# Optimization experiments

Measured on AMD Instinct MI355X. Metric: run time of the kernel, lower is better.

## Reference

```python
import jax, jax.numpy as jnp
import numpy as np

# Static problem sizes
REC = [5, 3, 6, 2]          # agents per scene (record_len), sum = 16
LMAX = max(REC)              # max cav count per group (static for padding)
C, H, W = 256, 96, 288       # feature channels and BEV spatial dims


def setup_inputs() -> dict:
    key = jax.random.key(0)
    total = sum(REC)
    x = jax.random.normal(key, (total, C, H, W), dtype=jnp.float32)
    record_len = jnp.array(REC, dtype=jnp.int32)
    return {"x": x, "record_len": record_len}


def _att_fusion(x, record_len):
    # x: (sum_cav, C, H, W); record_len: (B,)
    B = record_len.shape[0]
    Cdim, Hh, Ww = x.shape[1], x.shape[2], x.shape[3]
    P = Hh * Ww
    scale = 1.0 / np.sqrt(Cdim)

    # Pad ragged groups to (B, LMAX): row index into x, clamped + masked
    offsets = jnp.concatenate([jnp.zeros((1,), record_len.dtype),
                               jnp.cumsum(record_len)[:-1]])
    l = jnp.arange(LMAX)
    mask = l[None, :] < record_len[:, None]                       # (B, L)
    idx = offsets[:, None] + jnp.minimum(l[None, :], record_len[:, None] - 1)
    xf = x[idx].reshape(B, LMAX, Cdim, P)                         # (B, L, C, P)

    # Only the ego row (token 0) of the per-pixel self-attention is kept,
    # so compute attention for that single query per spatial location.
    q = xf[:, 0]                                                  # (B, C, P)
    scores = jnp.einsum('bcp,blcp->blp', q, xf) * scale           # (B, L, P)
    scores = jnp.where(mask[:, :, None], scores, jnp.float32(-1e9))
    attn = jax.nn.softmax(scores, axis=1)                         # over agents
    out = jnp.einsum('blp,blcp->bcp', attn, xf)                   # (B, C, P)
    return out.reshape(B, Cdim, Hh, Ww)


def reference(x, record_len):
    return _att_fusion(x, record_len)
```

## Files before the change

kernel.cpp:

```cpp
#include <hip/hip_runtime.h>


#define CC 256
#define PP (96 * 288)
#define P4 (PP / 4)
#define LMAXC 6
#define TPX 8
#define NGRP 32

template <int LEN>
__device__ __forceinline__ void att_body(
    const float4* __restrict__ xbase,
    float4* __restrict__ obase,
    float4 (&red)[LMAXC][NGRP][TPX],
    float4 (&sc)[LMAXC][TPX],
    float4 (&att)[LMAXC][TPX],
    int pxl, int grp, int tid)
{
    const size_t CP4 = (size_t)CC * P4;

    float4 xd[LEN][8];
#pragma unroll
    for (int ci = 0; ci < 8; ++ci) {
#pragma unroll
        for (int l = 0; l < LEN; ++l)
            xd[l][ci] = xbase[(size_t)l * CP4 + (size_t)ci * P4];
    }

    float4 s[LEN];
#pragma unroll
    for (int l = 0; l < LEN; ++l) s[l] = make_float4(0.f, 0.f, 0.f, 0.f);
#pragma unroll
    for (int ci = 0; ci < 8; ++ci) {
        const float4 x0 = xd[0][ci];
#pragma unroll
        for (int l = 0; l < LEN; ++l) {
            const float4 xl = xd[l][ci];
            s[l].x = fmaf(x0.x, xl.x, s[l].x);
            s[l].y = fmaf(x0.y, xl.y, s[l].y);
            s[l].z = fmaf(x0.z, xl.z, s[l].z);
            s[l].w = fmaf(x0.w, xl.w, s[l].w);
        }
    }

#pragma unroll
    for (int l = 0; l < LEN; ++l) red[l][grp][pxl] = s[l];
    __syncthreads();

    if (tid < 8 * LEN) {
        const int l = tid >> 3, px = tid & 7;
        float4 a = make_float4(0.f, 0.f, 0.f, 0.f);
#pragma unroll
        for (int g = 0; g < NGRP; ++g) {
            const float4 r = red[l][g][px];
            a.x += r.x; a.y += r.y; a.z += r.z; a.w += r.w;
        }
        sc[l][px] = make_float4(a.x * 0.0625f, a.y * 0.0625f,
                                a.z * 0.0625f, a.w * 0.0625f);
    }
    __syncthreads();

    if (tid < TPX) {
        float4 v[LEN];
#pragma unroll
        for (int l = 0; l < LEN; ++l) v[l] = sc[l][tid];
        float4 m = v[0];
#pragma unroll
        for (int l = 1; l < LEN; ++l) {
            m.x = fmaxf(m.x, v[l].x); m.y = fmaxf(m.y, v[l].y);
            m.z = fmaxf(m.z, v[l].z); m.w = fmaxf(m.w, v[l].w);
        }
        float4 sum = make_float4(0.f, 0.f, 0.f, 0.f);
#pragma unroll
        for (int l = 0; l < LEN; ++l) {
            v[l].x = __expf(v[l].x - m.x); sum.x += v[l].x;
            v[l].y = __expf(v[l].y - m.y); sum.y += v[l].y;
            v[l].z = __expf(v[l].z - m.z); sum.z += v[l].z;
            v[l].w = __expf(v[l].w - m.w); sum.w += v[l].w;
        }
        const float4 inv = make_float4(1.f / sum.x, 1.f / sum.y,
                                       1.f / sum.z, 1.f / sum.w);
#pragma unroll
        for (int l = 0; l < LEN; ++l)
            att[l][tid] = make_float4(v[l].x * inv.x, v[l].y * inv.y,
                                      v[l].z * inv.z, v[l].w * inv.w);
    }
    __syncthreads();

    float4 a[LEN];
#pragma unroll
    for (int l = 0; l < LEN; ++l) a[l] = att[l][pxl];

#pragma unroll
    for (int ci = 0; ci < 8; ++ci) {
        float4 acc;
        acc.x = a[0].x * xd[0][ci].x;
        acc.y = a[0].y * xd[0][ci].y;
        acc.z = a[0].z * xd[0][ci].z;
        acc.w = a[0].w * xd[0][ci].w;
#pragma unroll
        for (int l = 1; l < LEN; ++l) {
            acc.x = fmaf(a[l].x, xd[l][ci].x, acc.x);
            acc.y = fmaf(a[l].y, xd[l][ci].y, acc.y);
            acc.z = fmaf(a[l].z, xd[l][ci].z, acc.z);
            acc.w = fmaf(a[l].w, xd[l][ci].w, acc.w);
        }
        obase[(size_t)ci * P4] = acc;
    }
}

__global__ __launch_bounds__(256, 2) void attfusion_kernel(
    const float4* __restrict__ x, const int* __restrict__ rl,
    float4* __restrict__ out, int B)
{
    __shared__ float4 red[LMAXC][NGRP][TPX];
    __shared__ float4 sc[LMAXC][TPX];
    __shared__ float4 att[LMAXC][TPX];

    const int tid = threadIdx.x;
    const int pxl = tid & 7;
    const int grp = tid >> 3;

    const unsigned bid  = blockIdx.x;
    const int b    = bid % (unsigned)B;
    const int tile = bid / (unsigned)B;

    int off = 0;
    for (int i = 0; i < b; ++i) off += rl[i];
    int len = rl[b];
    if (len > LMAXC) len = LMAXC;
    if (len < 1)     len = 1;

    const size_t CP4 = (size_t)CC * P4;
    const int c0 = grp * 8;
    const float4* xbase = x   + (size_t)off * CP4 + (size_t)c0 * P4
                              + (size_t)tile * TPX + pxl;
    float4*       obase = out + (size_t)b   * CP4 + (size_t)c0 * P4
                              + (size_t)tile * TPX + pxl;

    switch (len) {
        case 1: att_body<1>(xbase, obase, red, sc, att, pxl, grp, tid); break;
        case 2: att_body<2>(xbase, obase, red, sc, att, pxl, grp, tid); break;
        case 3: att_body<3>(xbase, obase, red, sc, att, pxl, grp, tid); break;
        case 4: att_body<4>(xbase, obase, red, sc, att, pxl, grp, tid); break;
        case 5: att_body<5>(xbase, obase, red, sc, att, pxl, grp, tid); break;
        default: att_body<6>(xbase, obase, red, sc, att, pxl, grp, tid); break;
    }
}

extern "C" void kernel_launch(void* const* d_in, const int* in_sizes, int n_in,
                              void* d_out, int out_size, void* d_ws, size_t ws_size,
                              hipStream_t stream) {
    const float4* x   = (const float4*)d_in[0];
    const int*    rl  = (const int*)d_in[1];
    float4*       out = (float4*)d_out;
    const int B = in_sizes[1];
    dim3 grid((P4 / TPX) * B);
    attfusion_kernel<<<grid, 256, 0, stream>>>(x, rl, out, B);
}
```

Baseline: 644.1 us.

## Stream non-ego agents from memory twice to cut registers and raise occupancy

Only the ego agent's 8 channel vectors stay in registers. Each other agent is loaded once for the score pass and loaded again for the weighted-sum pass, instead of holding all LEN×8 float4 values live. The launch bounds rise from 2 to 4 blocks per SIMD, and output stores become nontemporal. This trades a second global read of the non-ego data, which may hit in cache, for much lower register pressure and more waves in flight to hide memory latency.

```diff
diff --git a/kernel.cpp b/kernel.cpp
--- a/kernel.cpp
+++ b/kernel.cpp
@@ -7,6 +7,8 @@
 #define LMAXC 6
 #define TPX 8
 #define NGRP 32
+
+typedef float f32x4 __attribute__((ext_vector_type(4)));
 
 template <int LEN>
 __device__ __forceinline__ void att_body(
@@ -19,28 +21,37 @@
 {
     const size_t CP4 = (size_t)CC * P4;
 
-    float4 xd[LEN][8];
+    float4 x0[8];
 #pragma unroll
-    for (int ci = 0; ci < 8; ++ci) {
-#pragma unroll
-        for (int l = 0; l < LEN; ++l)
-            xd[l][ci] = xbase[(size_t)l * CP4 + (size_t)ci * P4];
-    }
+    for (int ci = 0; ci < 8; ++ci) x0[ci] = xbase[(size_t)ci * P4];
 
     float4 s[LEN];
+    {
+        float4 a = make_float4(0.f, 0.f, 0.f, 0.f);
 #pragma unroll
-    for (int l = 0; l < LEN; ++l) s[l] = make_float4(0.f, 0.f, 0.f, 0.f);
+        for (int ci = 0; ci < 8; ++ci) {
+            a.x = fmaf(x0[ci].x, x0[ci].x, a.x);
+            a.y = fmaf(x0[ci].y, x0[ci].y, a.y);
+            a.z = fmaf(x0[ci].z, x0[ci].z, a.z);
+            a.w = fmaf(x0[ci].w, x0[ci].w, a.w);
+        }
+        s[0] = a;
+    }
 #pragma unroll
-    for (int ci = 0; ci < 8; ++ci) {
-        const float4 x0 = xd[0][ci];
+    for (int l = 1; l < LEN; ++l) {
+        float4 xl[8];
 #pragma unroll
-        for (int l = 0; l < LEN; ++l) {
-            const float4 xl = xd[l][ci];
-            s[l].x = fmaf(x0.x, xl.x, s[l].x);
-            s[l].y = fmaf(x0.y, xl.y, s[l].y);
-            s[l].z = fmaf(x0.z, xl.z, s[l].z);
-            s[l].w = fmaf(x0.w, xl.w, s[l].w);
+        for (int ci = 0; ci < 8; ++ci)
+            xl[ci] = xbase[(size_t)l * CP4 + (size_t)ci * P4];
+        float4 a = make_float4(0.f, 0.f, 0.f, 0.f);
+#pragma unroll
+        for (int ci = 0; ci < 8; ++ci) {
+            a.x = fmaf(x0[ci].x, xl[ci].x, a.x);
+            a.y = fmaf(x0[ci].y, xl[ci].y, a.y);
+            a.z = fmaf(x0[ci].z, xl[ci].z, a.z);
+            a.w = fmaf(x0[ci].w, xl[ci].w, a.w);
         }
+        s[l] = a;
     }
 
 #pragma unroll
@@ -91,25 +102,31 @@
 #pragma unroll
     for (int l = 0; l < LEN; ++l) a[l] = att[l][pxl];
 
+#pragma unroll 2
+    for (int ci = 0; ci < 8; ++ci) {
+        float4 xl[LEN > 1 ? LEN - 1 : 1];
 #pragma unroll
-    for (int ci = 0; ci < 8; ++ci) {
+        for (int l = 1; l < LEN; ++l)
+            xl[l - 1] = xbase[(size_t)l * CP4 + (size_t)ci * P4];
+
         float4 acc;
-        acc.x = a[0].x * xd[0][ci].x;
-        acc.y = a[0].y * xd[0][ci].y;
-        acc.z = a[0].z * xd[0][ci].z;
-        acc.w = a[0].w * xd[0][ci].w;
+        acc.x = a[0].x * x0[ci].x;
+        acc.y = a[0].y * x0[ci].y;
+        acc.z = a[0].z * x0[ci].z;
+        acc.w = a[0].w * x0[ci].w;
 #pragma unroll
         for (int l = 1; l < LEN; ++l) {
-            acc.x = fmaf(a[l].x, xd[l][ci].x, acc.x);
-            acc.y = fmaf(a[l].y, xd[l][ci].y, acc.y);
-            acc.z = fmaf(a[l].z, xd[l][ci].z, acc.z);
-            acc.w = fmaf(a[l].w, xd[l][ci].w, acc.w);
+            acc.x = fmaf(a[l].x, xl[l - 1].x, acc.x);
+            acc.y = fmaf(a[l].y, xl[l - 1].y, acc.y);
+            acc.z = fmaf(a[l].z, xl[l - 1].z, acc.z);
+            acc.w = fmaf(a[l].w, xl[l - 1].w, acc.w);
         }
-        obase[(size_t)ci * P4] = acc;
+        __builtin_nontemporal_store(*(const f32x4*)&acc,
+                                    (f32x4*)&obase[(size_t)ci * P4]);
     }
 }
 
-__global__ __launch_bounds__(256, 2) void attfusion_kernel(
+__global__ __launch_bounds__(256, 4) void attfusion_kernel(
     const float4* __restrict__ x, const int* __restrict__ rl,
     float4* __restrict__ out, int B)
 {
@@ -121,7 +138,7 @@
     const int pxl = tid & 7;
     const int grp = tid >> 3;
 
-    const unsigned bid  = blockIdx.x;
+    const unsigned bid = blockIdx.x;
     const int b    = bid % (unsigned)B;
     const int tile = bid / (unsigned)B;
 
```

Measured after the change: 718.8 us. +11.6%, slower.

## Cap register-resident agents at four, re-read extras, fuse softmax via shuffles

Applied to the files above, without the earlier changes.

Only up to four agents' channel slices stay in registers. Agents five and six are streamed from global memory for the score and read again in the output pass, which cuts register pressure for the larger templates. The separate softmax stage and its barrier are replaced by a single-wavefront reduction using xor shuffles across agent lanes, and the shared reduction buffer is padded. The cost is extra global reads for groups with more than four agents, which should mostly hit in cache.

```diff
diff --git a/kernel.cpp b/kernel.cpp
--- a/kernel.cpp
+++ b/kernel.cpp
@@ -7,83 +7,110 @@
 #define LMAXC 6
 #define TPX 8
 #define NGRP 32
+#define LSTRIDE 257
+
+__device__ __forceinline__ float4 shfl_xor4(float4 v, int mask) {
+    return make_float4(__shfl_xor(v.x, mask), __shfl_xor(v.y, mask),
+                       __shfl_xor(v.z, mask), __shfl_xor(v.w, mask));
+}
 
 template <int LEN>
 __device__ __forceinline__ void att_body(
     const float4* __restrict__ xbase,
     float4* __restrict__ obase,
-    float4 (&red)[LMAXC][NGRP][TPX],
-    float4 (&sc)[LMAXC][TPX],
+    float4* __restrict__ red,
     float4 (&att)[LMAXC][TPX],
     int pxl, int grp, int tid)
 {
+    constexpr int RES = (LEN < 4) ? LEN : 4;
     const size_t CP4 = (size_t)CC * P4;
 
-    float4 xd[LEN][8];
+    float4 xd[RES][8];
 #pragma unroll
-    for (int ci = 0; ci < 8; ++ci) {
+    for (int ci = 0; ci < 8; ++ci)
 #pragma unroll
-        for (int l = 0; l < LEN; ++l)
+        for (int l = 0; l < RES; ++l)
             xd[l][ci] = xbase[(size_t)l * CP4 + (size_t)ci * P4];
-    }
 
     float4 s[LEN];
+    {
+        float4 a = make_float4(0.f, 0.f, 0.f, 0.f);
 #pragma unroll
-    for (int l = 0; l < LEN; ++l) s[l] = make_float4(0.f, 0.f, 0.f, 0.f);
+        for (int ci = 0; ci < 8; ++ci) {
+            a.x = fmaf(xd[0][ci].x, xd[0][ci].x, a.x);
+            a.y = fmaf(xd[0][ci].y, xd[0][ci].y, a.y);
+            a.z = fmaf(xd[0][ci].z, xd[0][ci].z, a.z);
+            a.w = fmaf(xd[0][ci].w, xd[0][ci].w, a.w);
+        }
+        s[0] = a;
+    }
 #pragma unroll
-    for (int ci = 0; ci < 8; ++ci) {
-        const float4 x0 = xd[0][ci];
+    for (int l = 1; l < RES; ++l) {
+        float4 a = make_float4(0.f, 0.f, 0.f, 0.f);
 #pragma unroll
-        for (int l = 0; l < LEN; ++l) {
-            const float4 xl = xd[l][ci];
-            s[l].x = fmaf(x0.x, xl.x, s[l].x);
-            s[l].y = fmaf(x0.y, xl.y, s[l].y);
-            s[l].z = fmaf(x0.z, xl.z, s[l].z);
-            s[l].w = fmaf(x0.w, xl.w, s[l].w);
+        for (int ci = 0; ci < 8; ++ci) {
+            a.x = fmaf(xd[0][ci].x, xd[l][ci].x, a.x);
+            a.y = fmaf(xd[0][ci].y, xd[l][ci].y, a.y);
+            a.z = fmaf(xd[0][ci].z, xd[l][ci].z, a.z);
+            a.w = fmaf(xd[0][ci].w, xd[l][ci].w, a.w);
         }
+        s[l] = a;
+    }
+#pragma unroll
+    for (int l = RES; l < LEN; ++l) {
+        float4 xl[8];
+#pragma unroll
+        for (int ci = 0; ci < 8; ++ci)
+            xl[ci] = xbase[(size_t)l * CP4 + (size_t)ci * P4];
+        float4 a = make_float4(0.f, 0.f, 0.f, 0.f);
+#pragma unroll
+        for (int ci = 0; ci < 8; ++ci) {
+            a.x = fmaf(xd[0][ci].x, xl[ci].x, a.x);
+            a.y = fmaf(xd[0][ci].y, xl[ci].y, a.y);
+            a.z = fmaf(xd[0][ci].z, xl[ci].z, a.z);
+            a.w = fmaf(xd[0][ci].w, xl[ci].w, a.w);
+        }
+        s[l] = a;
     }
 
 #pragma unroll
-    for (int l = 0; l < LEN; ++l) red[l][grp][pxl] = s[l];
+    for (int l = 0; l < LEN; ++l) red[l * LSTRIDE + tid] = s[l];
     __syncthreads();
 
-    if (tid < 8 * LEN) {
+    if (tid < 64) {
         const int l = tid >> 3, px = tid & 7;
-        float4 a = make_float4(0.f, 0.f, 0.f, 0.f);
+        float4 v;
+        if (l < LEN) {
+            float4 a = make_float4(0.f, 0.f, 0.f, 0.f);
 #pragma unroll
-        for (int g = 0; g < NGRP; ++g) {
-            const float4 r = red[l][g][px];
-            a.x += r.x; a.y += r.y; a.z += r.z; a.w += r.w;
+            for (int g = 0; g < NGRP; ++g) {
+                const float4 r = red[l * LSTRIDE + g * 8 + px];
+                a.x += r.x; a.y += r.y; a.z += r.z; a.w += r.w;
+            }
+            v = make_float4(a.x * 0.0625f, a.y * 0.0625f,
+                            a.z * 0.0625f, a.w * 0.0625f);
+        } else {
+            v = make_float4(-1e9f, -1e9f, -1e9f, -1e9f);
         }
-        sc[l][px] = make_float4(a.x * 0.0625f, a.y * 0.0625f,
-                                a.z * 0.0625f, a.w * 0.0625f);
-    }
-    __syncthreads();
-
-    if (tid < TPX) {
-        float4 v[LEN];
+        float4 m = v;
 #pragma unroll
-        for (int l = 0; l < LEN; ++l) v[l] = sc[l][tid];
-        float4 m = v[0];
+        for (int mask = 8; mask <= 32; mask <<= 1) {
+            const float4 o = shfl_xor4(m, mask);
+            m.x = fmaxf(m.x, o.x); m.y = fmaxf(m.y, o.y);
+            m.z = fmaxf(m.z, o.z); m.w = fmaxf(m.w, o.w);
+        }
+        float4 e;
+        e.x = __expf(v.x - m.x); e.y = __expf(v.y - m.y);
+        e.z = __expf(v.z - m.z); e.w = __expf(v.w - m.w);
+        float4 sum = e;
 #pragma unroll
-        for (int l = 1; l < LEN; ++l) {
-            m.x = fmaxf(m.x, v[l].x); m.y = fmaxf(m.y, v[l].y);
-            m.z = fmaxf(m.z, v[l].z); m.w = fmaxf(m.w, v[l].w);
+        for (int mask = 8; mask <= 32; mask <<= 1) {
+            const float4 o = shfl_xor4(sum, mask);
+            sum.x += o.x; sum.y += o.y; sum.z += o.z; sum.w += o.w;
         }
-        float4 sum = make_float4(0.f, 0.f, 0.f, 0.f);
-#pragma unroll
-        for (int l = 0; l < LEN; ++l) {
-            v[l].x = __expf(v[l].x - m.x); sum.x += v[l].x;
-            v[l].y = __expf(v[l].y - m.y); sum.y += v[l].y;
-            v[l].z = __expf(v[l].z - m.z); sum.z += v[l].z;
-            v[l].w = __expf(v[l].w - m.w); sum.w += v[l].w;
-        }
-        const float4 inv = make_float4(1.f / sum.x, 1.f / sum.y,
-                                       1.f / sum.z, 1.f / sum.w);
-#pragma unroll
-        for (int l = 0; l < LEN; ++l)
-            att[l][tid] = make_float4(v[l].x * inv.x, v[l].y * inv.y,
-                                      v[l].z * inv.z, v[l].w * inv.w);
+        if (l < LEN)
+            att[l][px] = make_float4(e.x / sum.x, e.y / sum.y,
+                                     e.z / sum.z, e.w / sum.w);
     }
     __syncthreads();
 
@@ -99,11 +126,19 @@
         acc.z = a[0].z * xd[0][ci].z;
         acc.w = a[0].w * xd[0][ci].w;
 #pragma unroll
-        for (int l = 1; l < LEN; ++l) {
+        for (int l = 1; l < RES; ++l) {
             acc.x = fmaf(a[l].x, xd[l][ci].x, acc.x);
             acc.y = fmaf(a[l].y, xd[l][ci].y, acc.y);
             acc.z = fmaf(a[l].z, xd[l][ci].z, acc.z);
             acc.w = fmaf(a[l].w, xd[l][ci].w, acc.w);
+        }
+#pragma unroll
+        for (int l = RES; l < LEN; ++l) {
+            const float4 xl = xbase[(size_t)l * CP4 + (size_t)ci * P4];
+            acc.x = fmaf(a[l].x, xl.x, acc.x);
+            acc.y = fmaf(a[l].y, xl.y, acc.y);
+            acc.z = fmaf(a[l].z, xl.z, acc.z);
+            acc.w = fmaf(a[l].w, xl.w, acc.w);
         }
         obase[(size_t)ci * P4] = acc;
     }
@@ -113,15 +148,14 @@
     const float4* __restrict__ x, const int* __restrict__ rl,
     float4* __restrict__ out, int B)
 {
-    __shared__ float4 red[LMAXC][NGRP][TPX];
-    __shared__ float4 sc[LMAXC][TPX];
+    __shared__ float4 red[LMAXC * LSTRIDE];
     __shared__ float4 att[LMAXC][TPX];
 
     const int tid = threadIdx.x;
     const int pxl = tid & 7;
     const int grp = tid >> 3;
 
-    const unsigned bid  = blockIdx.x;
+    const unsigned bid = blockIdx.x;
     const int b    = bid % (unsigned)B;
     const int tile = bid / (unsigned)B;
 
@@ -139,12 +173,12 @@
                               + (size_t)tile * TPX + pxl;
 
     switch (len) {
-        case 1: att_body<1>(xbase, obase, red, sc, att, pxl, grp, tid); break;
-        case 2: att_body<2>(xbase, obase, red, sc, att, pxl, grp, tid); break;
-        case 3: att_body<3>(xbase, obase, red, sc, att, pxl, grp, tid); break;
-        case 4: att_body<4>(xbase, obase, red, sc, att, pxl, grp, tid); break;
-        case 5: att_body<5>(xbase, obase, red, sc, att, pxl, grp, tid); break;
-        default: att_body<6>(xbase, obase, red, sc, att, pxl, grp, tid); break;
+        case 1: att_body<1>(xbase, obase, red, att, pxl, grp, tid); break;
+        case 2: att_body<2>(xbase, obase, red, att, pxl, grp, tid); break;
+        case 3: att_body<3>(xbase, obase, red, att, pxl, grp, tid); break;
+        case 4: att_body<4>(xbase, obase, red, att, pxl, grp, tid); break;
+        case 5: att_body<5>(xbase, obase, red, att, pxl, grp, tid); break;
+        default: att_body<6>(xbase, obase, red, att, pxl, grp, tid); break;
     }
 }
 
```

After: 659.6 us. 1.02x slower.
